# Kernel tuning notes

Measured on AMD Instinct MI355X. Metric: run time of the kernel, lower is better.

## Reference

```python
import jax, jax.numpy as jnp
import numpy as np

B, S, H, E, K = 2, 2048, 1024, 8, 2
CAP_FACTOR = 1.5

def setup_inputs() -> dict:
    key = jax.random.key(0)
    ks = jax.random.split(key, 8)
    sd1 = 1.0 / np.sqrt(H)
    sd2 = 1.0 / np.sqrt(H + E)
    return {
        'hidden_states': jax.random.normal(ks[0], (B, S, H), dtype=jnp.float32),
        'w1': jax.random.normal(ks[1], (H, H), dtype=jnp.float32) * sd1,
        'b1': jnp.zeros((H,), jnp.float32),
        'w2': jax.random.normal(ks[2], (H, E), dtype=jnp.float32) * sd1,
        'b2': jnp.zeros((E,), jnp.float32),
        'wc1': jax.random.normal(ks[3], (H + E, H), dtype=jnp.float32) * sd2,
        'bc1': jnp.zeros((H,), jnp.float32),
        'wc2': jax.random.normal(ks[4], (H, E), dtype=jnp.float32) * sd1,
        'bc2': jnp.zeros((E,), jnp.float32),
        'cache_hit_rates': jax.random.uniform(ks[5], (E,), dtype=jnp.float32),
    }

def reference(hidden_states, w1, b1, w2, b2, wc1, bc1, wc2, bc2, cache_hit_rates):
    b, s, h = hidden_states.shape
    # router MLP: Linear -> ReLU -> Linear
    router_logits = jax.nn.relu(hidden_states @ w1 + b1) @ w2 + b2  # [B,S,E]
    # cache-aware adjustment
    avg_features = hidden_states.mean(axis=1)  # [B,H]
    combined = jnp.concatenate(
        [avg_features, jnp.broadcast_to(cache_hit_rates[None, :], (b, E))], axis=-1)
    adj = jnp.tanh(jax.nn.relu(combined @ wc1 + bc1) @ wc2 + bc2)  # [B,E]
    router_logits = router_logits + adj[:, None, :]
    router_probs = jax.nn.softmax(router_logits, axis=-1)  # [B,S,E]
    top_k_probs, top_k_indices = jax.lax.top_k(router_probs, K)  # [B,S,K]
    top_k_probs = top_k_probs / (top_k_probs.sum(axis=-1, keepdims=True) + 1e-8)
    capacity = int(b * s * CAP_FACTOR * K / E)
    # flatten in (b, s, k) order to replicate serial capacity counters
    N = b * s * K
    e_flat = top_k_indices.reshape(N)
    p_flat = top_k_probs.reshape(N)
    tok = jnp.arange(N) // K  # token index b*S+s
    onehot = jax.nn.one_hot(e_flat, E, dtype=jnp.int32)  # [N,E] small
    prior = jnp.cumsum(onehot, axis=0) - onehot  # exclusive count per expert
    pos = prior[jnp.arange(N), e_flat]  # slot within expert
    keep = pos < capacity
    posc = jnp.minimum(pos, capacity - 1)
    val = keep.astype(router_probs.dtype)
    dispatch = jnp.zeros((b * s, E, capacity), router_probs.dtype)
    dispatch = dispatch.at[tok, e_flat, posc].add(val).reshape(b, s, E, capacity)
    combine = jnp.zeros((b * s, E, capacity), router_probs.dtype)
    combine = combine.at[tok, e_flat, posc].add(val * p_flat).reshape(b, s, E, capacity)
    # load balancing aux loss
    router_prob_per_expert = router_probs.mean(axis=(0, 1))  # [E]
    expert_usage_rate = onehot.astype(router_probs.dtype).mean(axis=0)  # [E]
    aux_loss = jnp.sum(router_prob_per_expert * expert_usage_rate) * E
    return dispatch, combine, router_probs, aux_loss
```

## Files before the change

### kernel.cpp

```cpp
#include <hip/hip_runtime.h>
#include <hip/hip_bf16.h>

#define BB 2
#define SS 2048
#define HH 1024
#define EE 8
#define KK 2
#define CAP 1536
#define NTOK (BB * SS)
#define NASSIGN (NTOK * KK)

#define WS_PSUM   0
#define WS_AVG    8
#define WS_HC     2056
#define WS_ADJ    4104
#define WS_P1     4120
#define WS_P2     8216
#define WS_IDX    12312
#define WS_LOGITS 16408
#define WS_ZERO_FLOATS 4112
#define WS_ZERO_BYTES 16448
#define WS_BF16_BYTE 196704
#define WS_H_BYTE (WS_BF16_BYTE + 31457280)
#define WS_NEED (WS_H_BYTE + 16777216ull)

using short8 = __attribute__((ext_vector_type(8))) short;
using u16x8  = __attribute__((ext_vector_type(8))) unsigned short;
using f32x4  = __attribute__((ext_vector_type(4))) float;

__device__ __forceinline__ unsigned short f2bf(float f) {
  unsigned u = __float_as_uint(f);
  unsigned r = (u + 0x7fffu + ((u >> 16) & 1u)) >> 16;
  return (unsigned short)r;
}
__device__ __forceinline__ float bf2f(unsigned short h) {
  return __uint_as_float((unsigned)h << 16);
}
__device__ __forceinline__ void split2(float x, unsigned short& h,
                                       unsigned short& m) {
  h = f2bf(x);
  m = f2bf(x - bf2f(h));
}

__device__ __forceinline__ void gload_lds16(const void* g, void* l) {
  __builtin_amdgcn_global_load_lds(
      (const __attribute__((address_space(1))) void*)g,
      (__attribute__((address_space(3))) void*)l, 16, 0, 0);
}

#define PREPX_BLKS 4096
#define PREPW_BLKS 256
#define AVG_BLKS   128
__global__ __launch_bounds__(256) void k_prep(
    const float* __restrict__ x, const float* __restrict__ w1,
    unsigned short* __restrict__ Xh, unsigned short* __restrict__ Xm,
    unsigned short* __restrict__ Wh, unsigned short* __restrict__ Wm,
    float* __restrict__ wshead, float* __restrict__ avg_part) {
  __shared__ unsigned short Th[64 * 65], Tm[64 * 65];
  int tid = threadIdx.x;
  int bid = blockIdx.x;
  if (bid < PREPX_BLKS) {
    if (bid == 0)
      for (int j = tid; j < WS_ZERO_FLOATS; j += 256) wshead[j] = 0.f;
    int i = (bid * 256 + tid) * 4;
    float4 v = *(const float4*)&x[i];
    unsigned short h[4], m[4];
    split2(v.x, h[0], m[0]);
    split2(v.y, h[1], m[1]);
    split2(v.z, h[2], m[2]);
    split2(v.w, h[3], m[3]);
    *(ushort4*)&Xh[i] = make_ushort4(h[0], h[1], h[2], h[3]);
    *(ushort4*)&Xm[i] = make_ushort4(m[0], m[1], m[2], m[3]);
  } else if (bid < PREPX_BLKS + PREPW_BLKS) {
    int pid = bid - PREPX_BLKS;
    int k0 = (pid & 15) * 64, n0 = (pid >> 4) * 64;
    for (int i = 0; i < 16; ++i) {
      int e = i * 256 + tid;
      int k = e >> 6, n = e & 63;
      float v = w1[(size_t)(k0 + k) * HH + n0 + n];
      unsigned short h, m;
      split2(v, h, m);
      Th[n * 65 + k] = h; Tm[n * 65 + k] = m;
    }
    __syncthreads();
    for (int i = 0; i < 16; ++i) {
      int e = i * 256 + tid;
      int n = e >> 6, k = e & 63;
      size_t o = (size_t)(n0 + n) * HH + k0 + k;
      Wh[o] = Th[n * 65 + k]; Wm[o] = Tm[n * 65 + k];
    }
  } else {
    int pid = bid - PREPX_BLKS - PREPW_BLKS;
    int h = (pid & 3) * 256 + tid;
    int c = (pid >> 2) & 15;
    int b = pid >> 6;
    const float* p = x + (size_t)b * SS * HH + (size_t)(c * 128) * HH + h;
    float s = 0.f;
    for (int i = 0; i < 128; ++i) s += p[(size_t)i * HH];
    avg_part[(c * BB + b) * HH + h] = s;
  }
}

__global__ void k_avgp(const float* __restrict__ x, float* __restrict__ avg_part) {
  int h = blockIdx.x * 256 + threadIdx.x;
  int c = blockIdx.y;
  int b = blockIdx.z;
  const float* p = x + (size_t)b * SS * HH + (size_t)(c * 128) * HH + h;
  float s = 0.f;
  for (int i = 0; i < 128; ++i) s += p[(size_t)i * HH];
  avg_part[(c * BB + b) * HH + h] = s;
}

__global__ void k_hc(const float* __restrict__ avg_part, const float* __restrict__ chr,
                     const float* __restrict__ wc1, float* __restrict__ hc_raw) {
  __shared__ float avg_s[128];
  int tid = threadIdx.x;
  int j = blockIdx.x * 256 + tid;
  int c = blockIdx.y;
  int b = blockIdx.z;
  if (tid < 128) {
    float s = 0.f;
    for (int cc = 0; cc < 16; ++cc)
      s += avg_part[(cc * BB + b) * HH + c * 128 + tid];
    avg_s[tid] = s * (1.0f / SS);
  }
  __syncthreads();
  float acc = 0.f;
  for (int il = 0; il < 128; ++il)
    acc += avg_s[il] * wc1[(size_t)(c * 128 + il) * HH + j];
  if (c == 7)
    for (int i = 0; i < EE; ++i)
      acc += chr[i] * wc1[(size_t)(HH + i) * HH + j];
  atomicAdd(&hc_raw[b * HH + j], acc);
}

__global__ void k_adj(const float* __restrict__ hc_raw, const float* __restrict__ bc1,
                      const float* __restrict__ wc2, const float* __restrict__ bc2,
                      float* __restrict__ adj) {
  int b = blockIdx.x;
  int tid = threadIdx.x;
  float part[EE] = {};
  for (int j = tid; j < HH; j += 256) {
    float v = fmaxf(hc_raw[b * HH + j] + bc1[j], 0.f);
    for (int e = 0; e < EE; ++e) part[e] += v * wc2[j * EE + e];
  }
  for (int m = 1; m < 64; m <<= 1)
    for (int e = 0; e < EE; ++e) part[e] += __shfl_xor(part[e], m);
  __shared__ float red[4][EE];
  int wave = tid >> 6, lane = tid & 63;
  if (lane == 0)
    for (int e = 0; e < EE; ++e) red[wave][e] = part[e];
  __syncthreads();
  if (tid < EE) {
    float s = bc2[tid];
    for (int w = 0; w < 4; ++w) s += red[w][tid];
    adj[b * EE + tid] = tanhf(s);
  }
}

#define BM 128
#define BN 64
#define BK 64
#define NSLICE 32
#define ZF4_PER_BLOCK 49152
__global__ __launch_bounds__(256) void k_gemm_mfma(
    const unsigned short* __restrict__ Xh, const unsigned short* __restrict__ Xm,
    const unsigned short* __restrict__ Wh, const unsigned short* __restrict__ Wm,
    const float* __restrict__ b1, const float* __restrict__ w2,
    float* __restrict__ plg,
    f32x4* __restrict__ zout,
    const float* __restrict__ hc_raw, const float* __restrict__ bc1,
    const float* __restrict__ wc2, const float* __restrict__ bc2,
    float* __restrict__ adj) {
  __shared__ unsigned short As[2][BM * BK];
  __shared__ unsigned short Bs[2][BN * BK];
  __shared__ float b1s[BN];
  __shared__ float w2s[BN * 9];
  __shared__ float red[4][EE];
  int tid = threadIdx.x;

  if (blockIdx.y == HH / BN) {
    if (blockIdx.x >= BB) return;
    int b = blockIdx.x;
    float part[EE] = {};
    for (int j = tid; j < HH; j += 256) {
      float v = fmaxf(hc_raw[b * HH + j] + bc1[j], 0.f);
      for (int e = 0; e < EE; ++e) part[e] += v * wc2[j * EE + e];
    }
    for (int m = 1; m < 64; m <<= 1)
      for (int e = 0; e < EE; ++e) part[e] += __shfl_xor(part[e], m);
    int wave = tid >> 6, lane = tid & 63;
    if (lane == 0)
      for (int e = 0; e < EE; ++e) red[wave][e] = part[e];
    __syncthreads();
    if (tid < EE) {
      float s = bc2[tid];
      for (int w = 0; w < 4; ++w) s += red[w][tid];
      adj[b * EE + tid] = tanhf(s);
    }
    return;
  }

  int m0 = blockIdx.x * BM, n0 = blockIdx.y * BN;
  if (tid < BN) b1s[tid] = b1[n0 + tid];
#pragma unroll
  for (int rdx = 0; rdx < 2; ++rdx) {
    int i = tid + rdx * 256;
    int c = i >> 3, e = i & 7;
    w2s[c * 9 + e] = w2[(size_t)(n0 + c) * EE + e];
  }

  int bid = blockIdx.y * gridDim.x + blockIdx.x;
  f32x4* zp = zout + (size_t)bid * ZF4_PER_BLOCK;
  const f32x4 z4 = {0.f, 0.f, 0.f, 0.f};

  int lane = tid & 63, wave = tid >> 6;
  int wm = wave & 1, wn = wave >> 1;
  int q = lane >> 4, mr = lane & 15;
  int lr8 = lane >> 3;
  int lq8 = lane & 7;
  int lqs8 = lq8 ^ lr8;
  int mr7 = mr & 7;

  f32x4 acc[4][2] = {};
  const unsigned short* Ag[2] = {Xh, Xm};
  const unsigned short* Bg[2] = {Wh, Wm};

  for (int k0 = 0; k0 < HH; k0 += BK) {
    __syncthreads();
#pragma unroll
    for (int j = 0; j < 8; ++j) {
      int i = wave + 4 * j;
      int s = i >> 4;
      int rem = i & 15;
      int g = rem >> 1, h = rem & 1;
      gload_lds16(Ag[s] + (size_t)(m0 + g * 16 + h * 8 + lr8) * HH + k0 + lqs8 * 8,
                  &As[s][g * 1024 + h * 512]);
    }
#pragma unroll
    for (int j = 0; j < 4; ++j) {
      int i = wave + 4 * j;
      int s = i >> 3;
      int rem = i & 7;
      int g = rem >> 1, h = rem & 1;
      gload_lds16(Bg[s] + (size_t)(n0 + g * 16 + h * 8 + lr8) * HH + k0 + lqs8 * 8,
                  &Bs[s][g * 1024 + h * 512]);
    }
    __syncthreads();

    {
      int ki = k0 >> 6;
      f32x4* zb = zp + ki * (256 * 12) + tid;
#pragma unroll
      for (int j = 0; j < 12; ++j) __builtin_nontemporal_store(z4, &zb[j * 256]);
    }

#pragma unroll
    for (int kk = 0; kk < 2; ++kk) {
      short8 af[2][4], bv[2][2];
#pragma unroll
      for (int s = 0; s < 2; ++s) {
#pragma unroll
        for (int mi = 0; mi < 4; ++mi)
          af[s][mi] = *(const short8*)
              &As[s][(wm * 4 + mi) * 1024 + mr * 64 + ((kk * 4 + q) ^ mr7) * 8];
#pragma unroll
        for (int ni = 0; ni < 2; ++ni)
          bv[s][ni] = *(const short8*)
              &Bs[s][(wn * 2 + ni) * 1024 + mr * 64 + ((kk * 4 + q) ^ mr7) * 8];
      }
#pragma unroll
      for (int mi = 0; mi < 4; ++mi)
#pragma unroll
        for (int ni = 0; ni < 2; ++ni) {
          f32x4 c = acc[mi][ni];
          c = __builtin_amdgcn_mfma_f32_16x16x32_bf16(af[0][mi], bv[0][ni], c, 0, 0, 0);
          c = __builtin_amdgcn_mfma_f32_16x16x32_bf16(af[0][mi], bv[1][ni], c, 0, 0, 0);
          c = __builtin_amdgcn_mfma_f32_16x16x32_bf16(af[1][mi], bv[0][ni], c, 0, 0, 0);
          c = __builtin_amdgcn_mfma_f32_16x16x32_bf16(af[1][mi], bv[1][ni], c, 0, 0, 0);
          acc[mi][ni] = c;
        }
    }
  }

  int slice = blockIdx.y * 2 + wn;
#pragma unroll
  for (int mi = 0; mi < 4; ++mi)
#pragma unroll
    for (int r = 0; r < 4; ++r) {
      int rowl = wm * 64 + mi * 16 + q * 4 + r;
      int c0 = wn * 32 + mr, c1 = c0 + 16;
      float v0 = fmaxf(acc[mi][0][r] + b1s[c0], 0.f);
      float v1 = fmaxf(acc[mi][1][r] + b1s[c1], 0.f);
      float pe[EE];
#pragma unroll
      for (int e = 0; e < EE; ++e)
        pe[e] = v0 * w2s[c0 * 9 + e] + v1 * w2s[c1 * 9 + e];
#pragma unroll
      for (int m = 1; m < 16; m <<= 1)
#pragma unroll
        for (int e = 0; e < EE; ++e) pe[e] += __shfl_xor(pe[e], m);
      if (mr == 0) {
        float* lp = &plg[((size_t)slice * NTOK + (m0 + rowl)) * EE];
        float4 pa = {pe[0], pe[1], pe[2], pe[3]};
        float4 pb = {pe[4], pe[5], pe[6], pe[7]};
        *(float4*)lp = pa;
        *(float4*)(lp + 4) = pb;
      }
    }
}

__global__ __launch_bounds__(256) void k_logits2(
    const float* __restrict__ plg, const float* __restrict__ b2,
    const float* __restrict__ adj, float* __restrict__ probs_out,
    int* __restrict__ idx_pack, float* __restrict__ p1o, float* __restrict__ p2o,
    float* __restrict__ psum) {
  __shared__ float ps[EE];
  int tid = threadIdx.x;
  if (tid < EE) ps[tid] = 0.f;
  __syncthreads();
  int t = blockIdx.x * 256 + tid;
  int b = t >> 11;
  float l[EE] = {};
#pragma unroll
  for (int s = 0; s < NSLICE; ++s) {
    const float* pp = &plg[((size_t)s * NTOK + t) * EE];
    float4 a = *(const float4*)pp;
    float4 c = *(const float4*)(pp + 4);
    l[0] += a.x; l[1] += a.y; l[2] += a.z; l[3] += a.w;
    l[4] += c.x; l[5] += c.y; l[6] += c.z; l[7] += c.w;
  }
  float mx = -1e30f;
#pragma unroll
  for (int e = 0; e < EE; ++e) {
    l[e] += b2[e] + adj[b * EE + e];
    mx = fmaxf(mx, l[e]);
  }
  float s = 0.f;
#pragma unroll
  for (int e = 0; e < EE; ++e) { l[e] = expf(l[e] - mx); s += l[e]; }
  float inv = 1.f / s;
#pragma unroll
  for (int e = 0; e < EE; ++e) l[e] *= inv;
  float4 pa = {l[0], l[1], l[2], l[3]}, pb = {l[4], l[5], l[6], l[7]};
  *(float4*)&probs_out[(size_t)t * EE] = pa;
  *(float4*)&probs_out[(size_t)t * EE + 4] = pb;
  int e1 = 0; float p1 = l[0];
#pragma unroll
  for (int e = 1; e < EE; ++e) if (l[e] > p1) { p1 = l[e]; e1 = e; }
  int e2 = -1; float p2 = -1.f;
#pragma unroll
  for (int e = 0; e < EE; ++e) if (e != e1 && l[e] > p2) { p2 = l[e]; e2 = e; }
  float norm = 1.f / (p1 + p2 + 1e-8f);
  idx_pack[t] = e1 | (e2 << 8);
  p1o[t] = p1 * norm;
  p2o[t] = p2 * norm;
#pragma unroll
  for (int m = 1; m < 64; m <<= 1)
#pragma unroll
    for (int e = 0; e < EE; ++e) l[e] += __shfl_xor(l[e], m);
  if ((tid & 63) == 0)
#pragma unroll
    for (int e = 0; e < EE; ++e) atomicAdd(&ps[e], l[e]);
  __syncthreads();
  if (tid < EE) atomicAdd(&psum[tid], ps[tid]);
}

__global__ __launch_bounds__(256) void k_gemm_f32(
    const float* __restrict__ X, const float* __restrict__ w1,
    const float* __restrict__ b1, const float* __restrict__ w2,
    float* __restrict__ logits) {
  __shared__ float Asf[16][65];
  __shared__ float Bsf[16][64];
  __shared__ float w2sf[64][EE];
  int tid = threadIdx.x;
  int m0 = blockIdx.x * 64, n0 = blockIdx.y * 64;
  for (int i = tid; i < 64 * EE; i += 256)
    w2sf[i / EE][i % EE] = w2[(size_t)(n0 + i / EE) * EE + (i % EE)];
  float acc[4][4] = {};
  int tx = tid & 15, ty = tid >> 4;
  for (int k0 = 0; k0 < HH; k0 += 16) {
    for (int idx = tid; idx < 64 * 16; idx += 256) {
      int m = idx >> 4, kk = idx & 15;
      Asf[kk][m] = X[(size_t)(m0 + m) * HH + k0 + kk];
    }
    for (int idx = tid; idx < 16 * 64; idx += 256) {
      int kk = idx >> 6, n = idx & 63;
      Bsf[kk][n] = w1[(size_t)(k0 + kk) * HH + n0 + n];
    }
    __syncthreads();
    for (int kk = 0; kk < 16; ++kk) {
      float a[4], bb[4];
      for (int i = 0; i < 4; ++i) a[i] = Asf[kk][ty * 4 + i];
      for (int j = 0; j < 4; ++j) bb[j] = Bsf[kk][tx * 4 + j];
      for (int i = 0; i < 4; ++i)
        for (int j = 0; j < 4; ++j) acc[i][j] += a[i] * bb[j];
    }
    __syncthreads();
  }
  float p[4][EE] = {};
  for (int i = 0; i < 4; ++i)
    for (int j = 0; j < 4; ++j) {
      int c = tx * 4 + j;
      float v = fmaxf(acc[i][j] + b1[n0 + c], 0.f);
      for (int e = 0; e < EE; ++e) p[i][e] += v * w2sf[c][e];
    }
  for (int m = 1; m < 16; m <<= 1)
    for (int i = 0; i < 4; ++i)
      for (int e = 0; e < EE; ++e) p[i][e] += __shfl_xor(p[i][e], m);
  if (tx == 0)
    for (int i = 0; i < 4; ++i)
      for (int e = 0; e < EE; ++e)
        atomicAdd(&logits[(size_t)(m0 + ty * 4 + i) * EE + e], p[i][e]);
}

__global__ void k_init_logits(const float* __restrict__ adj, const float* __restrict__ b2,
                              float* __restrict__ logits) {
  int i = blockIdx.x * 256 + threadIdx.x;
  int e = i & 7;
  int t = i >> 3;
  int b = t >> 11;
  logits[i] = b2[e] + adj[b * EE + e];
}

__global__ void k_softmax(const float* __restrict__ logits, float* __restrict__ probs_out,
                          int* __restrict__ idx_pack, float* __restrict__ p1o,
                          float* __restrict__ p2o, float* __restrict__ psum) {
  int t = blockIdx.x * 256 + threadIdx.x;
  float l[EE];
  float mx = -1e30f;
  for (int e = 0; e < EE; ++e) { l[e] = logits[t * EE + e]; mx = fmaxf(mx, l[e]); }
  float s = 0.f;
  for (int e = 0; e < EE; ++e) { l[e] = expf(l[e] - mx); s += l[e]; }
  float inv = 1.f / s;
  for (int e = 0; e < EE; ++e) { l[e] *= inv; probs_out[t * EE + e] = l[e]; }
  int e1 = 0; float p1 = l[0];
  for (int e = 1; e < EE; ++e) if (l[e] > p1) { p1 = l[e]; e1 = e; }
  int e2 = -1; float p2 = -1.f;
  for (int e = 0; e < EE; ++e) if (e != e1 && l[e] > p2) { p2 = l[e]; e2 = e; }
  float norm = 1.f / (p1 + p2 + 1e-8f);
  idx_pack[t] = e1 | (e2 << 8);
  p1o[t] = p1 * norm;
  p2o[t] = p2 * norm;
  for (int m = 1; m < 64; m <<= 1)
    for (int e = 0; e < EE; ++e) l[e] += __shfl_xor(l[e], m);
  if ((threadIdx.x & 63) == 0)
    for (int e = 0; e < EE; ++e) atomicAdd(&psum[e], l[e]);
}

__global__ __launch_bounds__(256) void k_route(
    const int* __restrict__ idx_pack, const float* __restrict__ p1,
    const float* __restrict__ p2, const float* __restrict__ psum,
    float* __restrict__ disp, float* __restrict__ comb, float* __restrict__ aux_out) {
  __shared__ int cnt[256][EE];
  __shared__ int tot[EE];
  int tid = threadIdx.x;
  const int CH = NASSIGN / 256;
  int n0 = tid * CH;
  int local[EE] = {};
  for (int n = n0; n < n0 + CH; ++n) {
    int t = n >> 1;
    int pk = idx_pack[t];
    int e = (n & 1) ? (pk >> 8) : (pk & 0xff);
    local[e]++;
  }
  for (int e = 0; e < EE; ++e) cnt[tid][e] = local[e];
  __syncthreads();
  if (tid < EE) {
    int run = 0;
    for (int t = 0; t < 256; ++t) { int v = cnt[t][tid]; cnt[t][tid] = run; run += v; }
    tot[tid] = run;
  }
  __syncthreads();
  int off[EE];
  for (int e = 0; e < EE; ++e) off[e] = cnt[tid][e];
  for (int n = n0; n < n0 + CH; ++n) {
    int t = n >> 1;
    int pk = idx_pack[t];
    int e; float p;
    if (n & 1) { e = pk >> 8; p = p2[t]; } else { e = pk & 0xff; p = p1[t]; }
    int pos = off[e]++;
    if (pos < CAP) {
      size_t o = (size_t)t * EE * CAP + (size_t)e * CAP + pos;
      disp[o] = 1.0f;
      comb[o] = p;
    }
  }
  if (tid == 0) {
    float aux = 0.f;
    for (int e = 0; e < EE; ++e)
      aux += (psum[e] / (float)NTOK) * ((float)tot[e] / (float)NASSIGN);
    aux_out[0] = aux * (float)EE;
  }
}

extern "C" void kernel_launch(void* const* d_in, const int* in_sizes, int n_in,
                              void* d_out, int out_size, void* d_ws, size_t ws_size,
                              hipStream_t stream) {
  const float* x   = (const float*)d_in[0];
  const float* w1  = (const float*)d_in[1];
  const float* b1  = (const float*)d_in[2];
  const float* w2  = (const float*)d_in[3];
  const float* b2  = (const float*)d_in[4];
  const float* wc1 = (const float*)d_in[5];
  const float* bc1 = (const float*)d_in[6];
  const float* wc2 = (const float*)d_in[7];
  const float* bc2 = (const float*)d_in[8];
  const float* chr = (const float*)d_in[9];

  float* out = (float*)d_out;
  float* disp  = out;
  float* comb  = disp + (size_t)NTOK * EE * CAP;
  float* probs = comb + (size_t)NTOK * EE * CAP;
  float* aux   = probs + (size_t)NTOK * EE;

  float* ws = (float*)d_ws;
  float* psum   = ws + WS_PSUM;
  float* hcr    = ws + WS_HC;
  float* adj    = ws + WS_ADJ;
  float* p1     = ws + WS_P1;
  float* p2     = ws + WS_P2;
  int*   idxp   = (int*)(ws + WS_IDX);
  float* logits = ws + WS_LOGITS;
  float* avgp   = ws + WS_LOGITS;

  char* wsb = (char*)d_ws;
  unsigned short* Xh = (unsigned short*)(wsb + WS_BF16_BYTE);
  unsigned short* Xm = Xh + (size_t)NTOK * HH;
  unsigned short* Wh = Xm + (size_t)NTOK * HH;
  unsigned short* Wm = Wh + (size_t)HH * HH;
  float* plg = (float*)(wsb + WS_H_BYTE);

  bool use_mfma = ws_size >= WS_NEED;

  if (use_mfma) {
    k_prep<<<PREPX_BLKS + PREPW_BLKS + AVG_BLKS, 256, 0, stream>>>(
        x, w1, Xh, Xm, Wh, Wm, ws, avgp);
    k_hc<<<dim3(HH / 256, 8, BB), 256, 0, stream>>>(avgp, chr, wc1, hcr);
    k_gemm_mfma<<<dim3(NTOK / BM, HH / BN + 1), 256, 0, stream>>>(
        Xh, Xm, Wh, Wm, b1, w2, plg, (f32x4*)d_out,
        hcr, bc1, wc2, bc2, adj);
    k_logits2<<<NTOK / 256, 256, 0, stream>>>(plg, b2, adj, probs, idxp, p1, p2, psum);
  } else {
    hipMemsetAsync(d_ws, 0, WS_ZERO_BYTES, stream);
    hipMemsetAsync(d_out, 0, (size_t)out_size * sizeof(float), stream);
    k_avgp<<<dim3(HH / 256, 16, BB), 256, 0, stream>>>(x, avgp);
    k_hc<<<dim3(HH / 256, 8, BB), 256, 0, stream>>>(avgp, chr, wc1, hcr);
    k_adj<<<BB, 256, 0, stream>>>(hcr, bc1, wc2, bc2, adj);
    k_init_logits<<<(NTOK * EE) / 256, 256, 0, stream>>>(adj, b2, logits);
    k_gemm_f32<<<dim3(NTOK / 64, HH / 64), 256, 0, stream>>>(x, w1, b1, w2, logits);
    k_softmax<<<NTOK / 256, 256, 0, stream>>>(logits, probs, idxp, p1, p2, psum);
  }
  k_route<<<1, 256, 0, stream>>>(idxp, p1, p2, psum, disp, comb, aux);
}
```

Baseline: 491.6 us.

## Parallelize capacity routing with per-block expert histograms and block-level scan

The logits kernel now records a per-block histogram of top-2 expert choices. A new 16-block routing kernel takes an exclusive prefix over earlier blocks' histograms plus an in-block serial scan to assign capacity slots, replacing the single-block serial router. This spreads routing across more blocks. The cost is an extra histogram buffer and a serial per-expert scan over 256 threads in each block.

```diff
diff --git a/kernel.cpp b/kernel.cpp
--- a/kernel.cpp
+++ b/kernel.cpp
@@ -314,10 +314,11 @@
     const float* __restrict__ plg, const float* __restrict__ b2,
     const float* __restrict__ adj, float* __restrict__ probs_out,
     int* __restrict__ idx_pack, float* __restrict__ p1o, float* __restrict__ p2o,
-    float* __restrict__ psum) {
+    float* __restrict__ psum, int* __restrict__ hist) {
   __shared__ float ps[EE];
-  int tid = threadIdx.x;
-  if (tid < EE) ps[tid] = 0.f;
+  __shared__ int hs[EE];
+  int tid = threadIdx.x;
+  if (tid < EE) { ps[tid] = 0.f; hs[tid] = 0; }
   __syncthreads();
   int t = blockIdx.x * 256 + tid;
   int b = t >> 11;
@@ -355,6 +356,8 @@
   idx_pack[t] = e1 | (e2 << 8);
   p1o[t] = p1 * norm;
   p2o[t] = p2 * norm;
+  atomicAdd(&hs[e1], 1);
+  atomicAdd(&hs[e2], 1);
 #pragma unroll
   for (int m = 1; m < 64; m <<= 1)
 #pragma unroll
@@ -363,7 +366,60 @@
 #pragma unroll
     for (int e = 0; e < EE; ++e) atomicAdd(&ps[e], l[e]);
   __syncthreads();
-  if (tid < EE) atomicAdd(&psum[tid], ps[tid]);
+  if (tid < EE) {
+    atomicAdd(&psum[tid], ps[tid]);
+    hist[blockIdx.x * EE + tid] = hs[tid];
+  }
+}
+
+__global__ __launch_bounds__(256) void k_route3(
+    const int* __restrict__ idx_pack, const float* __restrict__ p1,
+    const float* __restrict__ p2, const int* __restrict__ hist,
+    const float* __restrict__ psum,
+    float* __restrict__ disp, float* __restrict__ comb,
+    float* __restrict__ aux_out) {
+  __shared__ int cnt[256][EE];
+  int tid = threadIdx.x;
+  int c = blockIdx.x;
+  int t = c * 256 + tid;
+  int pk = idx_pack[t];
+  int e1 = pk & 0xff, e2 = pk >> 8;
+  int local[EE] = {};
+  local[e1]++; local[e2]++;
+#pragma unroll
+  for (int e = 0; e < EE; ++e) cnt[tid][e] = local[e];
+  __syncthreads();
+  if (tid < EE) {
+    int run = 0;
+    for (int cc = 0; cc < c; ++cc) run += hist[cc * EE + tid];
+    for (int th = 0; th < 256; ++th) {
+      int v = cnt[th][tid];
+      cnt[th][tid] = run;
+      run += v;
+    }
+  }
+  __syncthreads();
+  int pos1 = cnt[tid][e1];
+  int pos2 = cnt[tid][e2];
+  if (pos1 < CAP) {
+    size_t o = (size_t)t * EE * CAP + (size_t)e1 * CAP + pos1;
+    disp[o] = 1.0f;
+    comb[o] = p1[t];
+  }
+  if (pos2 < CAP) {
+    size_t o = (size_t)t * EE * CAP + (size_t)e2 * CAP + pos2;
+    disp[o] = 1.0f;
+    comb[o] = p2[t];
+  }
+  if (c == 0 && tid == 0) {
+    float aux = 0.f;
+    for (int e = 0; e < EE; ++e) {
+      int tot = 0;
+      for (int cc = 0; cc < 16; ++cc) tot += hist[cc * EE + e];
+      aux += (psum[e] / (float)NTOK) * ((float)tot / (float)NASSIGN);
+    }
+    aux_out[0] = aux * (float)EE;
+  }
 }
 
 __global__ __launch_bounds__(256) void k_gemm_f32(
@@ -529,7 +585,8 @@
   unsigned short* Xm = Xh + (size_t)NTOK * HH;
   unsigned short* Wh = Xm + (size_t)NTOK * HH;
   unsigned short* Wm = Wh + (size_t)HH * HH;
-  float* plg = (float*)(wsb + WS_H_BYTE);
+  float* plg  = (float*)(wsb + WS_H_BYTE);
+  int*   hist = (int*)(wsb + WS_H_BYTE + 4194304);
 
   bool use_mfma = ws_size >= WS_NEED;
 
@@ -540,7 +597,9 @@
     k_gemm_mfma<<<dim3(NTOK / BM, HH / BN + 1), 256, 0, stream>>>(
         Xh, Xm, Wh, Wm, b1, w2, plg, (f32x4*)d_out,
         hcr, bc1, wc2, bc2, adj);
-    k_logits2<<<NTOK / 256, 256, 0, stream>>>(plg, b2, adj, probs, idxp, p1, p2, psum);
+    k_logits2<<<NTOK / 256, 256, 0, stream>>>(plg, b2, adj, probs, idxp, p1, p2,
+                                              psum, hist);
+    k_route3<<<16, 256, 0, stream>>>(idxp, p1, p2, hist, psum, disp, comb, aux);
   } else {
     hipMemsetAsync(d_ws, 0, WS_ZERO_BYTES, stream);
     hipMemsetAsync(d_out, 0, (size_t)out_size * sizeof(float), stream);
@@ -550,6 +609,6 @@
     k_init_logits<<<(NTOK * EE) / 256, 256, 0, stream>>>(adj, b2, logits);
     k_gemm_f32<<<dim3(NTOK / 64, HH / 64), 256, 0, stream>>>(x, w1, b1, w2, logits);
     k_softmax<<<NTOK / 256, 256, 0, stream>>>(logits, probs, idxp, p1, p2, psum);
-  }
-  k_route<<<1, 256, 0, stream>>>(idxp, p1, p2, psum, disp, comb, aux);
-}
+    k_route<<<1, 256, 0, stream>>>(idxp, p1, p2, psum, disp, comb, aux);
+  }
+}
```

New measurement: 476.8 us. 3.0% less time.
